# Performance work log

Hardware: AMD Instinct MI355X
Metric: run time of the kernel (lower is better)

The kernel has to match this reference:

```python
import jax, jax.numpy as jnp
import numpy as np
from jax import lax

D_MODEL = 256
N_LAYERS = 4
D_STATE = 64
EXPAND = 2
HEADDIM = 64
D_CONV = 4
D_INNER = EXPAND * D_MODEL                      # 512
NHEADS = D_INNER // HEADDIM                     # 8
CONV_DIM = D_INNER + 2 * D_STATE                # 640 (ngroups=1)
D_IN_PROJ = 2 * D_INNER + 2 * D_STATE + NHEADS  # 1160
B_SZ, SEQ = 8, 2048


def _silu(x):
    return x * jax.nn.sigmoid(x)


def _mamba2(u, W_in, W_conv, b_conv, dt_bias, A_log, Dp, norm_w, W_out):
    # Standard Mamba2 block (in_proj -> causal depthwise conv -> selective scan
    # with per-head scalar A -> gated RMSNorm -> out_proj).
    B, L, _ = u.shape
    zxbcdt = u @ W_in.T                                   # [B,L,1160]
    z = zxbcdt[..., :D_INNER]
    xBC = zxbcdt[..., D_INNER:D_INNER + CONV_DIM]
    dt = jax.nn.softplus(zxbcdt[..., D_INNER + CONV_DIM:] + dt_bias)  # [B,L,H]
    # causal depthwise conv1d + silu
    xc = lax.conv_general_dilated(xBC.transpose(0, 2, 1), W_conv[:, None, :],
                                  (1,), [(D_CONV - 1, 0)],
                                  dimension_numbers=('NCH', 'OIH', 'NCH'),
                                  feature_group_count=CONV_DIM)
    xBC = _silu(xc.transpose(0, 2, 1) + b_conv)
    x = xBC[..., :D_INNER].reshape(B, L, NHEADS, HEADDIM)
    Bm = xBC[..., D_INNER:D_INNER + D_STATE]              # [B,L,N]
    Cm = xBC[..., D_INNER + D_STATE:]                     # [B,L,N]
    dA = jnp.exp(dt * (-jnp.exp(A_log)))                  # [B,L,H]

    def step(h, inp):
        dA_t, dt_t, x_t, B_t, C_t = inp
        # h: [B,H,P,N]
        h = dA_t[:, :, None, None] * h + (dt_t[:, :, None] * x_t)[..., None] * B_t[:, None, None, :]
        y = jnp.einsum('bhpn,bn->bhp', h, C_t)
        return h, y

    h0 = jnp.zeros((B, NHEADS, HEADDIM, D_STATE), u.dtype)
    xs = (dA.transpose(1, 0, 2), dt.transpose(1, 0, 2), x.transpose(1, 0, 2, 3),
          Bm.transpose(1, 0, 2), Cm.transpose(1, 0, 2))
    _, ys = lax.scan(step, h0, xs)                        # [L,B,H,P]
    y = ys.transpose(1, 0, 2, 3) + Dp[None, None, :, None] * x
    y = y.reshape(B, L, D_INNER)
    y = y * _silu(z)                                      # gate before RMSNorm
    y = y * lax.rsqrt(jnp.mean(y * y, axis=-1, keepdims=True) + 1e-5) * norm_w
    return y @ W_out.T


def _encoder(x, pf, pb):
    for i in range(N_LAYERS - 1):
        y_fwd = _mamba2(x, *[p[i] for p in pf])
        y_bwd = _mamba2(x[:, ::-1], *[p[i] for p in pb])[:, ::-1]
        x = y_fwd + y_bwd
    h_fwd = _mamba2(x, *[p[-1] for p in pf])
    h_bwd = _mamba2(x[:, ::-1], *[p[-1] for p in pb])[:, ::-1]
    H = (h_fwd + h_bwd).mean(axis=1)
    return h_fwd, h_bwd, H


def _make_params(key):
    k = jax.random.split(key, 4)
    W_in = jax.random.normal(k[0], (N_LAYERS, D_IN_PROJ, D_MODEL), jnp.float32) * 0.02
    W_conv = jax.random.normal(k[1], (N_LAYERS, CONV_DIM, D_CONV), jnp.float32) * 0.2
    b_conv = jnp.zeros((N_LAYERS, CONV_DIM), jnp.float32)
    dt = jnp.exp(jax.random.uniform(k[2], (N_LAYERS, NHEADS)) * (np.log(0.1) - np.log(0.001)) + np.log(0.001))
    dt_bias = dt + jnp.log(-jnp.expm1(-dt))               # softplus^{-1}(dt)
    A_log = jnp.log(jax.random.uniform(k[3], (N_LAYERS, NHEADS), minval=1.0, maxval=16.0))
    Dp = jnp.ones((N_LAYERS, NHEADS), jnp.float32)
    norm_w = jnp.ones((N_LAYERS, D_INNER), jnp.float32)
    W_out = jax.random.normal(jax.random.fold_in(k[0], 7), (N_LAYERS, D_MODEL, D_INNER), jnp.float32) * 0.02
    return (W_in, W_conv, b_conv, dt_bias, A_log, Dp, norm_w, W_out)


def setup_inputs():
    key = jax.random.key(0)
    kx, kf, kb = jax.random.split(key, 3)
    x = jax.random.normal(kx, (B_SZ, SEQ, D_MODEL), jnp.float32)
    pf = _make_params(kf)
    pb = _make_params(kb)
    names = ['Win', 'Wconv', 'bconv', 'dt_bias', 'A_log', 'D', 'norm_w', 'Wout']
    inp = {'x_conditioned': x}
    for n, p in zip(names, pf):
        inp[n + '_f'] = p
    for n, p in zip(names, pb):
        inp[n + '_b'] = p
    return inp


def reference(x_conditioned, Win_f, Wconv_f, bconv_f, dt_bias_f, A_log_f, D_f, norm_w_f, Wout_f,
              Win_b, Wconv_b, bconv_b, dt_bias_b, A_log_b, D_b, norm_w_b, Wout_b):
    pf = (Win_f, Wconv_f, bconv_f, dt_bias_f, A_log_f, D_f, norm_w_f, Wout_f)
    pb = (Win_b, Wconv_b, bconv_b, dt_bias_b, A_log_b, D_b, norm_w_b, Wout_b)
    return _encoder(x_conditioned, pf, pb)
```

## Files before the change

### kernel.cpp

```cpp
#include <hip/hip_runtime.h>
#include <math.h>


#define TC 64
#define NC 32
#define SPITCH 72

#define ZB_STR   8388608u
#define XBCB_STR 10485760u
#define HINPU_STR 8388608u
#define XCP_STR  10485760u
#define DT_STR   131072u
#define SB_STR   131072u
#define PT_STR   2048u

typedef __attribute__((ext_vector_type(4))) float f32x4;
typedef __attribute__((ext_vector_type(8))) short s16x8;

#define MFMA __builtin_amdgcn_mfma_f32_16x16x32_bf16

__device__ __forceinline__ float siluf(float x) { return x / (1.f + expf(-x)); }

__device__ __forceinline__ ushort f2b(float f) {
  union { float f; uint u; } v; v.f = f;
  return (ushort)((v.u + 0x7FFFu + ((v.u >> 16) & 1u)) >> 16);
}
__device__ __forceinline__ float b2f(ushort u) {
  union { uint u; float f; } v; v.u = ((uint)u) << 16; return v.f;
}
__device__ __forceinline__ int swz(int r, int c) { return c ^ (r & 3) ^ ((r >> 2) & 3); }

__device__ __forceinline__ int soff(int base, int r, int cc) {
  return base + r * SPITCH + ((((cc >> 3) ^ (r & 7) ^ ((r >> 3) & 7)) << 3) | (cc & 7));
}
__device__ __forceinline__ int toff(int base, int r, int cc) {
  return base + r * 64 + ((((cc >> 3) ^ (r & 7)) << 3) | (cc & 7));
}

__device__ __forceinline__ uint packf(float y) {
  const ushort hb = f2b(y);
  const ushort lb = f2b(y - b2f(hb));
  return (uint)hb | ((uint)lb << 16);
}
__device__ __forceinline__ float unpackf(uint u) {
  return b2f((ushort)(u & 0xffffu)) + b2f((ushort)(u >> 16));
}

__device__ __forceinline__ void unzip8(const uint4 u0, const uint4 u1, s16x8& hh, s16x8& ll) {
  const uint a[8] = {u0.x, u0.y, u0.z, u0.w, u1.x, u1.y, u1.z, u1.w};
#pragma unroll
  for (int e = 0; e < 8; ++e) {
    hh[e] = (short)(a[e] & 0xffffu);
    ll[e] = (short)(a[e] >> 16);
  }
}

__device__ __forceinline__ void stage16p(ushort* tiles, const uint* src,
                                         int bh_, int bl_, int r, int c0) {
  const uint4 u0 = *(const uint4*)(src + c0);
  const uint4 u1 = *(const uint4*)(src + c0 + 4);
  const uint4 u2 = *(const uint4*)(src + c0 + 8);
  const uint4 u3 = *(const uint4*)(src + c0 + 12);
  s16x8 h0, l0, h1, l1;
  unzip8(u0, u1, h0, l0);
  unzip8(u2, u3, h1, l1);
  *(s16x8*)&tiles[toff(bh_, r, c0)]     = h0;
  *(s16x8*)&tiles[toff(bl_, r, c0)]     = l0;
  *(s16x8*)&tiles[toff(bh_, r, c0 + 8)] = h1;
  *(s16x8*)&tiles[toff(bl_, r, c0 + 8)] = l1;
}

__global__ __launch_bounds__(256) void k_cvt(
    const float* __restrict__ src, ushort* __restrict__ dst, int n8)
{
  const int i = blockIdx.x * 256 + threadIdx.x;
  if (i >= n8) return;
  const float4 v0 = *(const float4*)(src + (size_t)i * 8);
  const float4 v1 = *(const float4*)(src + (size_t)i * 8 + 4);
  s16x8 h;
#pragma unroll
  for (int e = 0; e < 4; ++e) h[e] = (short)f2b(((const float*)&v0)[e]);
#pragma unroll
  for (int e = 0; e < 4; ++e) h[e + 4] = (short)f2b(((const float*)&v1)[e]);
  *(s16x8*)(dst + (size_t)i * 8) = h;
}

__global__ __launch_bounds__(256) void k_gemmb(
    const ushort* __restrict__ A, const ushort* __restrict__ Winb, int layer,
    ushort* __restrict__ zb, ushort* __restrict__ xbc,
    const float* __restrict__ db0, const float* __restrict__ db1,
    const float* __restrict__ Al0, const float* __restrict__ Al1,
    float* __restrict__ dtb, float* __restrict__ dab)
{
  const int zd = blockIdx.z;
  const ushort* W = Winb + ((size_t)zd * 4 + layer) * 296960;
  zb  += (size_t)zd * ZB_STR;
  xbc += (size_t)zd * XBCB_STR;
  dtb += (size_t)zd * DT_STR;
  dab += (size_t)zd * DT_STR;
  const float* dt_bias = zd ? db1 : db0;
  const float* A_log   = zd ? Al1 : Al0;
  const int N = 1160, K = 256;

  __shared__ __align__(16) ushort lds[17408];
  const int tid = threadIdx.x;
  const int lane = tid & 63;
  const int wid = tid >> 6;
  const int wr = wid >> 1, wc = wid & 1;
  const int m0 = blockIdx.x * 128, n0 = blockIdx.y * 128;

  const int tr = tid >> 1;
  const int th = tid & 1;
  const int gm = m0 + tr;
  const int bb = gm >> 11, tt = gm & 2047;
  const int tphys = zd ? (2047 - tt) : tt;
  const ushort* Arow = A + (size_t)((bb << 11) + tphys) * 256 + th * 16;
  const int wn = n0 + tr;
  const ushort* Wrow = (wn < N) ? (W + (size_t)wn * K + th * 16) : nullptr;

  const int asw0 = tr * 32 + swz(tr, th * 2) * 8;
  const int asw1 = tr * 32 + swz(tr, th * 2 + 1) * 8;

  f32x4 acc[4][4];
#pragma unroll
  for (int i = 0; i < 4; ++i)
#pragma unroll
    for (int j = 0; j < 4; ++j) acc[i][j] = (f32x4){0.f, 0.f, 0.f, 0.f};

  int aoff[4], boff[4];
#pragma unroll
  for (int f = 0; f < 4; ++f) {
    const int ar = wr * 64 + f * 16 + (lane & 15);
    aoff[f] = ar * 32 + swz(ar, lane >> 4) * 8;
    const int br = wc * 64 + f * 16 + (lane & 15);
    boff[f] = 4096 + br * 32 + swz(br, lane >> 4) * 8;
  }

  const s16x8 zz = (s16x8){0, 0, 0, 0, 0, 0, 0, 0};
  s16x8 a0 = *(const s16x8*)(Arow);
  s16x8 a1 = *(const s16x8*)(Arow + 8);
  s16x8 b0 = zz, b1 = zz;
  if (Wrow) {
    b0 = *(const s16x8*)(Wrow);
    b1 = *(const s16x8*)(Wrow + 8);
  }

  for (int k0 = 0; k0 < K; k0 += 32) {
    __syncthreads();
    *(s16x8*)&lds[asw0] = a0;
    *(s16x8*)&lds[asw1] = a1;
    *(s16x8*)&lds[4096 + asw0] = b0;
    *(s16x8*)&lds[4096 + asw1] = b1;
    __syncthreads();
    if (k0 + 32 < K) {
      a0 = *(const s16x8*)(Arow + k0 + 32);
      a1 = *(const s16x8*)(Arow + k0 + 40);
      if (Wrow) {
        b0 = *(const s16x8*)(Wrow + k0 + 32);
        b1 = *(const s16x8*)(Wrow + k0 + 40);
      }
    }
    s16x8 af[4], bf[4];
#pragma unroll
    for (int f = 0; f < 4; ++f) {
      af[f] = *(const s16x8*)&lds[aoff[f]];
      bf[f] = *(const s16x8*)&lds[boff[f]];
    }
#pragma unroll
    for (int i = 0; i < 4; ++i)
#pragma unroll
      for (int j = 0; j < 4; ++j)
        acc[i][j] = MFMA(af[i], bf[j], acc[i][j], 0, 0, 0);
  }

  const int by = blockIdx.y;
  if (by == 9) {
    if (wc == 0 && (lane & 15) < 8) {
      const int cl = lane & 15;
      const float bias = dt_bias[cl];
      const float eAl = expf(A_log[cl]);
#pragma unroll
      for (int i = 0; i < 4; ++i) {
        const int r = m0 + wr * 64 + i * 16 + (lane >> 4) * 4;
#pragma unroll
        for (int g = 0; g < 4; ++g) {
          const float v = acc[i][0][g] + bias;
          const float sp = (v > 20.f) ? v : log1pf(expf(v));
          dtb[(size_t)(r + g) * 8 + cl] = sp;
          dab[(size_t)(r + g) * 8 + cl] = sp * eAl;
        }
      }
    }
    return;
  }
  __syncthreads();
#pragma unroll
  for (int i = 0; i < 4; ++i) {
    const int r = wr * 64 + i * 16 + (lane >> 4) * 4;
#pragma unroll
    for (int j = 0; j < 4; ++j) {
      const int ccol = wc * 64 + j * 16 + (lane & 15);
#pragma unroll
      for (int g = 0; g < 4; ++g)
        lds[(r + g) * 136 + ccol] = f2b(acc[i][j][g]);
    }
  }
  __syncthreads();
  const int rr = tid >> 1, hf = tid & 1;
  const int grow = m0 + rr;
  ushort* dst; int stride, colb;
  if (by < 4) { dst = zb;  stride = 512; colb = n0; }
  else        { dst = xbc; stride = 640; colb = n0 - 512; }
  ushort* dp = dst + (size_t)grow * stride + colb + hf * 64;
  const ushort* sp = &lds[rr * 136 + hf * 64];
#pragma unroll
  for (int q = 0; q < 8; ++q)
    *(s16x8*)(dp + q * 8) = *(const s16x8*)(sp + q * 8);
}

__global__ __launch_bounds__(256) void k_gemmo_mid(
    const ushort* __restrict__ ybf, const ushort* __restrict__ Woutb, int layer,
    ushort* __restrict__ xbf)
{
  __shared__ __align__(16) ushort lds[8192];
  const int tid = threadIdx.x;
  const int lane = tid & 63;
  const int wid = tid >> 6;
  const int wr = wid >> 1, wc = wid & 1;
  const int m0 = blockIdx.x * 128, n0 = blockIdx.y * 128;

  const int tr = tid >> 1;
  const int th = tid & 1;
  const int gm = m0 + tr;
  const int bb = gm >> 11, tt = gm & 2047;
  const int wn = n0 + tr;

  const int asw0 = tr * 32 + swz(tr, th * 2) * 8;
  const int asw1 = tr * 32 + swz(tr, th * 2 + 1) * 8;

  f32x4 acc[4][4];
#pragma unroll
  for (int i = 0; i < 4; ++i)
#pragma unroll
    for (int j = 0; j < 4; ++j) acc[i][j] = (f32x4){0.f, 0.f, 0.f, 0.f};

  int aoff[4], boff[4];
#pragma unroll
  for (int f = 0; f < 4; ++f) {
    const int ar = wr * 64 + f * 16 + (lane & 15);
    aoff[f] = ar * 32 + swz(ar, lane >> 4) * 8;
    const int br = wc * 64 + f * 16 + (lane & 15);
    boff[f] = 4096 + br * 32 + swz(br, lane >> 4) * 8;
  }

  for (int dir = 0; dir < 2; ++dir) {
    const int tphys = dir ? (2047 - tt) : tt;
    const ushort* Arow = ybf + (size_t)dir * ZB_STR
                       + (size_t)((bb << 11) + tphys) * 512 + th * 16;
    const ushort* Wrow = Woutb + ((size_t)dir * 4 + layer) * 131072
                       + (size_t)wn * 512 + th * 16;
    s16x8 a0 = *(const s16x8*)(Arow);
    s16x8 a1 = *(const s16x8*)(Arow + 8);
    s16x8 b0 = *(const s16x8*)(Wrow);
    s16x8 b1 = *(const s16x8*)(Wrow + 8);
    for (int k0 = 0; k0 < 512; k0 += 32) {
      __syncthreads();
      *(s16x8*)&lds[asw0] = a0;
      *(s16x8*)&lds[asw1] = a1;
      *(s16x8*)&lds[4096 + asw0] = b0;
      *(s16x8*)&lds[4096 + asw1] = b1;
      __syncthreads();
      if (k0 + 32 < 512) {
        a0 = *(const s16x8*)(Arow + k0 + 32);
        a1 = *(const s16x8*)(Arow + k0 + 40);
        b0 = *(const s16x8*)(Wrow + k0 + 32);
        b1 = *(const s16x8*)(Wrow + k0 + 40);
      }
      s16x8 af[4], bf[4];
#pragma unroll
      for (int f = 0; f < 4; ++f) {
        af[f] = *(const s16x8*)&lds[aoff[f]];
        bf[f] = *(const s16x8*)&lds[boff[f]];
      }
#pragma unroll
      for (int i = 0; i < 4; ++i)
#pragma unroll
        for (int j = 0; j < 4; ++j)
          acc[i][j] = MFMA(af[i], bf[j], acc[i][j], 0, 0, 0);
    }
  }

#pragma unroll
  for (int i = 0; i < 4; ++i) {
    const int rb = m0 + wr * 64 + i * 16 + (lane >> 4) * 4;
#pragma unroll
    for (int g = 0; g < 4; ++g) {
      const size_t rbase = (size_t)(rb + g) * 256 + n0 + wc * 64 + (lane & 15);
#pragma unroll
      for (int j = 0; j < 4; ++j)
        xbf[rbase + j * 16] = f2b(acc[i][j][g]);
    }
  }
}

__global__ __launch_bounds__(256) void k_gemmo_last(
    const ushort* __restrict__ ybf, const ushort* __restrict__ Woutb,
    float* __restrict__ hF, float* __restrict__ hB)
{
  const int zd = blockIdx.z;
  const ushort* A = ybf + (size_t)zd * ZB_STR;
  const ushort* W = Woutb + ((size_t)zd * 4 + 3) * 131072;
  float* Cout = zd ? hB : hF;

  __shared__ __align__(16) ushort lds[8192];
  const int tid = threadIdx.x;
  const int lane = tid & 63;
  const int wid = tid >> 6;
  const int wr = wid >> 1, wc = wid & 1;
  const int m0 = blockIdx.x * 128, n0 = blockIdx.y * 128;

  const int tr = tid >> 1;
  const int th = tid & 1;
  const int gm = m0 + tr;
  const ushort* Arow = A + (size_t)gm * 512 + th * 16;
  const int wn = n0 + tr;
  const ushort* Wrow = W + (size_t)wn * 512 + th * 16;

  const int asw0 = tr * 32 + swz(tr, th * 2) * 8;
  const int asw1 = tr * 32 + swz(tr, th * 2 + 1) * 8;

  f32x4 acc[4][4];
#pragma unroll
  for (int i = 0; i < 4; ++i)
#pragma unroll
    for (int j = 0; j < 4; ++j) acc[i][j] = (f32x4){0.f, 0.f, 0.f, 0.f};

  int aoff[4], boff[4];
#pragma unroll
  for (int f = 0; f < 4; ++f) {
    const int ar = wr * 64 + f * 16 + (lane & 15);
    aoff[f] = ar * 32 + swz(ar, lane >> 4) * 8;
    const int br = wc * 64 + f * 16 + (lane & 15);
    boff[f] = 4096 + br * 32 + swz(br, lane >> 4) * 8;
  }

  s16x8 a0 = *(const s16x8*)(Arow);
  s16x8 a1 = *(const s16x8*)(Arow + 8);
  s16x8 b0 = *(const s16x8*)(Wrow);
  s16x8 b1 = *(const s16x8*)(Wrow + 8);

  for (int k0 = 0; k0 < 512; k0 += 32) {
    __syncthreads();
    *(s16x8*)&lds[asw0] = a0;
    *(s16x8*)&lds[asw1] = a1;
    *(s16x8*)&lds[4096 + asw0] = b0;
    *(s16x8*)&lds[4096 + asw1] = b1;
    __syncthreads();
    if (k0 + 32 < 512) {
      a0 = *(const s16x8*)(Arow + k0 + 32);
      a1 = *(const s16x8*)(Arow + k0 + 40);
      b0 = *(const s16x8*)(Wrow + k0 + 32);
      b1 = *(const s16x8*)(Wrow + k0 + 40);
    }
    s16x8 af[4], bf[4];
#pragma unroll
    for (int f = 0; f < 4; ++f) {
      af[f] = *(const s16x8*)&lds[aoff[f]];
      bf[f] = *(const s16x8*)&lds[boff[f]];
    }
#pragma unroll
    for (int i = 0; i < 4; ++i)
#pragma unroll
      for (int j = 0; j < 4; ++j)
        acc[i][j] = MFMA(af[i], bf[j], acc[i][j], 0, 0, 0);
  }

#pragma unroll
  for (int i = 0; i < 4; ++i) {
    const int rb = m0 + wr * 64 + i * 16 + (lane >> 4) * 4;
#pragma unroll
    for (int g = 0; g < 4; ++g) {
      const int row = rb + g;
      const int b2_ = row >> 11, t2 = row & 2047;
      const int tw = zd ? (2047 - t2) : t2;
      float* crow = Cout + ((size_t)((b2_ << 11) + tw)) * 256 + n0 + wc * 64 + (lane & 15);
#pragma unroll
      for (int j = 0; j < 4; ++j)
        crow[j * 16] = acc[i][j][g];
    }
  }
}

__global__ __launch_bounds__(256) void k_conv(
    const ushort* __restrict__ xbc,
    const float* __restrict__ Wc0, const float* __restrict__ Wc1,
    const float* __restrict__ bc0, const float* __restrict__ bc1,
    uint* __restrict__ xcp)
{
  const int zd = blockIdx.z;
  xbc += (size_t)zd * XBCB_STR;
  xcp += (size_t)zd * XCP_STR;
  const float* Wc = zd ? Wc1 : Wc0;
  const float* bc = zd ? bc1 : bc0;

  const int t = threadIdx.x;
  const int cg = blockIdx.x * 8 + (t & 7);
  const int c0 = cg * 8;
  const int rt0 = (blockIdx.y * 32 + (t >> 3)) * 16;

  float4 wv[8];
  const float4* wp = (const float4*)(Wc + c0 * 4);
#pragma unroll
  for (int e = 0; e < 8; ++e) wv[e] = wp[e];
  float bias[8];
#pragma unroll
  for (int e = 0; e < 8; ++e) bias[e] = bc[c0 + e];

  const s16x8 zz = (s16x8){0, 0, 0, 0, 0, 0, 0, 0};
  s16x8 w0, w1, w2;
  {
    const int l0 = rt0 & 2047;
    w0 = (l0 >= 3) ? *(const s16x8*)(xbc + (size_t)(rt0 - 3) * 640 + c0) : zz;
    w1 = (l0 >= 2) ? *(const s16x8*)(xbc + (size_t)(rt0 - 2) * 640 + c0) : zz;
    w2 = (l0 >= 1) ? *(const s16x8*)(xbc + (size_t)(rt0 - 1) * 640 + c0) : zz;
  }

#pragma unroll 4
  for (int i = 0; i < 16; ++i) {
    const int row = rt0 + i;
    const s16x8 cur = *(const s16x8*)(xbc + (size_t)row * 640 + c0);
    uint o[8];
#pragma unroll
    for (int e = 0; e < 8; ++e) {
      const float* w = (const float*)&wv[e];
      float a = bias[e];
      a = fmaf(b2f((ushort)w0[e]), w[0], a);
      a = fmaf(b2f((ushort)w1[e]), w[1], a);
      a = fmaf(b2f((ushort)w2[e]), w[2], a);
      a = fmaf(b2f((ushort)cur[e]), w[3], a);
      o[e] = packf(siluf(a));
    }
    uint* op = xcp + (size_t)row * 640 + c0;
    *(uint4*)op = make_uint4(o[0], o[1], o[2], o[3]);
    *(uint4*)(op + 4) = make_uint4(o[4], o[5], o[6], o[7]);
    w0 = w1; w1 = w2; w2 = cur;
  }
}

__global__ __launch_bounds__(256) void k_scan1(
    uint* __restrict__ xcp, const float* __restrict__ dt,
    const float* __restrict__ dtA,
    const float* __restrict__ Dp0, const float* __restrict__ Dp1,
    uint* __restrict__ hin, float* __restrict__ Sbuf,
    float* __restrict__ PT)
{
  const int zd = blockIdx.z;
  xcp  += (size_t)zd * XCP_STR;
  dt   += (size_t)zd * DT_STR;
  dtA  += (size_t)zd * DT_STR;
  hin  += (size_t)zd * HINPU_STR;
  Sbuf += (size_t)zd * SB_STR;
  PT   += (size_t)zd * PT_STR;
  const float* Dp = zd ? Dp1 : Dp0;

  const int c = blockIdx.x & (NC - 1);
  const int bhi = blockIdx.x >> 5;
  const int b = bhi >> 3, h = bhi & 7;
  const int tid = threadIdx.x;
  const int lane = tid & 63;
  const int wid = tid >> 6;
  const int r0 = b * 2048 + c * TC;
  const int hbase = h * 64;
  __shared__ __align__(16) ushort tiles[24576];
  __shared__ float Ssh[64], dtsh[64], vsh[64];
  enum { PCH = 0, PCL = 4096, PBH = 8192, PBL = 12288, PXH = 16384, PXL = 20480 };

  if (tid < 64) {
    float a = dtA[(size_t)(r0 + tid) * 8 + h];
    const float d = dt[(size_t)(r0 + tid) * 8 + h];
#pragma unroll
    for (int off = 1; off < 64; off <<= 1) {
      const float t = __shfl_up(a, off);
      if (tid >= off) a += t;
    }
    const float slast = __shfl(a, 63);
    Ssh[tid] = a;
    dtsh[tid] = d;
    vsh[tid] = expf(a - slast) * d;
    Sbuf[(size_t)bhi * 2048 + c * TC + tid] = a;
    if (tid == 63) PT[bhi * NC + c] = expf(-slast);
  }
  {
    const int r = tid >> 2, c0 = (tid & 3) * 16;
    const uint* rowp = xcp + (size_t)(r0 + r) * 640;
    stage16p(tiles, rowp + 512, PBH, PBL, r, c0);
    stage16p(tiles, rowp + 576, PCH, PCL, r, c0);
    stage16p(tiles, rowp + hbase, PXH, PXL, r, c0);
  }
  __syncthreads();

  const int ib = wid * 16;
  const int frow = lane & 15;
  const int fkc = lane >> 4;

  const int tp = tid >> 2;
  const int tj0 = (tid & 3) * 16;
  s16x8 xtr[4], btr[4];
#pragma unroll
  for (int cc = 0; cc < 2; ++cc) {
    const int j0 = tj0 + cc * 8;
    s16x8 vh, vl, wh, wl;
#pragma unroll
    for (int e = 0; e < 8; ++e) {
      const int ax = toff(PXH, j0 + e, tp);
      vh[e] = (short)tiles[ax];
      vl[e] = (short)tiles[ax + 4096];
      const int ab = toff(PBH, j0 + e, tp);
      wh[e] = (short)tiles[ab];
      wl[e] = (short)tiles[ab + 4096];
    }
    xtr[cc] = vh; xtr[cc + 2] = vl;
    btr[cc] = wh; btr[cc + 2] = wl;
  }

  s16x8 pah[2], pal[2];
#pragma unroll
  for (int ks = 0; ks < 2; ++ks) {
    pah[ks] = *(const s16x8*)&tiles[toff(PCH, ib + frow, ks * 32 + fkc * 8)];
    pal[ks] = *(const s16x8*)&tiles[toff(PCL, ib + frow, ks * 32 + fkc * 8)];
  }
  f32x4 acc[4];
#pragma unroll
  for (int jt = 0; jt < 4; ++jt) acc[jt] = (f32x4){0.f, 0.f, 0.f, 0.f};
#pragma unroll
  for (int jt = 0; jt < 4; ++jt) {
#pragma unroll
    for (int ks = 0; ks < 2; ++ks) {
      const s16x8 tbh = *(const s16x8*)&tiles[toff(PBH, jt * 16 + frow, ks * 32 + fkc * 8)];
      const s16x8 tbl = *(const s16x8*)&tiles[toff(PBL, jt * 16 + frow, ks * 32 + fkc * 8)];
      acc[jt] = MFMA(pah[ks], tbh, acc[jt], 0, 0, 0);
      acc[jt] = MFMA(pah[ks], tbl, acc[jt], 0, 0, 0);
      acc[jt] = MFMA(pal[ks], tbh, acc[jt], 0, 0, 0);
    }
  }
  float Si[4];
#pragma unroll
  for (int g = 0; g < 4; ++g) Si[g] = Ssh[ib + fkc * 4 + g];
#pragma unroll
  for (int jt = 0; jt < 4; ++jt) {
    const int j = jt * 16 + frow;
    const float Sj = Ssh[j], dj = dtsh[j];
#pragma unroll
    for (int g = 0; g < 4; ++g) {
      const int i = ib + fkc * 4 + g;
      const float w = (j <= i) ? __expf(Sj - Si[g]) * dj : 0.f;
      const float gt = acc[jt][g] * w;
      const ushort gh = f2b(gt);
      tiles[toff(PCH, i, j)] = gh;
      tiles[toff(PCL, i, j)] = f2b(gt - b2f(gh));
    }
  }
  __syncthreads();

#pragma unroll
  for (int cc = 0; cc < 2; ++cc) {
    *(s16x8*)&tiles[toff(PXH, tp, tj0 + cc * 8)] = xtr[cc];
    *(s16x8*)&tiles[toff(PXL, tp, tj0 + cc * 8)] = xtr[cc + 2];
    *(s16x8*)&tiles[toff(PBH, tp, tj0 + cc * 8)] = btr[cc];
    *(s16x8*)&tiles[toff(PBL, tp, tj0 + cc * 8)] = btr[cc + 2];
  }
  __syncthreads();

  s16x8 gah[2], gal[2];
#pragma unroll
  for (int ks = 0; ks < 2; ++ks) {
    gah[ks] = *(const s16x8*)&tiles[toff(PCH, ib + frow, ks * 32 + fkc * 8)];
    gal[ks] = *(const s16x8*)&tiles[toff(PCL, ib + frow, ks * 32 + fkc * 8)];
  }
  const float dpv = Dp[h];
#pragma unroll
  for (int pt = 0; pt < 4; ++pt) {
    f32x4 accY = (f32x4){0.f, 0.f, 0.f, 0.f};
#pragma unroll
    for (int ks = 0; ks < 2; ++ks) {
      const s16x8 xh = *(const s16x8*)&tiles[toff(PXH, pt * 16 + frow, ks * 32 + fkc * 8)];
      const s16x8 xl = *(const s16x8*)&tiles[toff(PXL, pt * 16 + frow, ks * 32 + fkc * 8)];
      accY = MFMA(gah[ks], xh, accY, 0, 0, 0);
      accY = MFMA(gah[ks], xl, accY, 0, 0, 0);
      accY = MFMA(gal[ks], xh, accY, 0, 0, 0);
    }
    const int p = pt * 16 + frow;
#pragma unroll
    for (int g = 0; g < 4; ++g) {
      const int i = ib + fkc * 4 + g;
      const int ax = toff(PXH, p, i);
      const float xv = b2f(tiles[ax]) + b2f(tiles[ax + 4096]);
      xcp[(size_t)(r0 + i) * 640 + hbase + p] = packf(accY[g] + dpv * xv);
    }
  }

  s16x8 xvh[2], xvl[2];
#pragma unroll
  for (int ks = 0; ks < 2; ++ks) {
    const int J0 = ks * 32 + fkc * 8;
    const s16x8 xh = *(const s16x8*)&tiles[toff(PXH, ib + frow, J0)];
    const s16x8 xl = *(const s16x8*)&tiles[toff(PXL, ib + frow, J0)];
#pragma unroll
    for (int e = 0; e < 8; ++e) {
      const float xf = (b2f((ushort)xh[e]) + b2f((ushort)xl[e])) * vsh[J0 + e];
      const ushort nh = f2b(xf);
      xvh[ks][e] = (short)nh;
      xvl[ks][e] = (short)f2b(xf - b2f(nh));
    }
  }
  uint* hbp = hin + (((size_t)(bhi * NC + c)) << 12);
#pragma unroll
  for (int nt = 0; nt < 4; ++nt) {
    f32x4 accC = (f32x4){0.f, 0.f, 0.f, 0.f};
#pragma unroll
    for (int ks = 0; ks < 2; ++ks) {
      const s16x8 tbh = *(const s16x8*)&tiles[toff(PBH, nt * 16 + frow, ks * 32 + fkc * 8)];
      const s16x8 tbl = *(const s16x8*)&tiles[toff(PBL, nt * 16 + frow, ks * 32 + fkc * 8)];
      accC = MFMA(xvh[ks], tbh, accC, 0, 0, 0);
      accC = MFMA(xvh[ks], tbl, accC, 0, 0, 0);
      accC = MFMA(xvl[ks], tbh, accC, 0, 0, 0);
    }
    const int n = nt * 16 + frow;
    const int kss = nt >> 1;
    const int nlo3 = (n >> 3) & 3, ne = n & 7;
#pragma unroll
    for (int g = 0; g < 4; ++g) {
      const int plo = fkc * 4 + g;
      const int off = ((wid * 2 + kss) << 9) + (nlo3 * 16 + plo) * 8 + ne;
      hbp[off] = packf(accC[g]);
    }
  }
}

__global__ __launch_bounds__(256) void k_scan2(
    uint* __restrict__ hin, const float* __restrict__ PT)
{
  const int zd = blockIdx.z;
  hin += (size_t)zd * HINPU_STR;
  PT  += (size_t)zd * PT_STR;
  const int bh = blockIdx.x >> 2, jt = blockIdx.x & 3;
  const int t = threadIdx.x;
  float hv[4] = {0.f, 0.f, 0.f, 0.f};
  for (int c = 0; c < NC; ++c) {
    uint* base = hin + (((size_t)(bh * NC + c)) << 12) + (jt << 10) + t * 4;
    const float pt = PT[bh * NC + c];
    const uint4 u = *(const uint4*)base;
    const float vals[4] = {unpackf(u.x), unpackf(u.y), unpackf(u.z), unpackf(u.w)};
    uint4 nv;
    uint* nvp = (uint*)&nv;
#pragma unroll
    for (int k = 0; k < 4; ++k) {
      const float old = hv[k];
      hv[k] = fmaf(pt, hv[k], vals[k]);
      nvp[k] = packf(old);
    }
    *(uint4*)base = nv;
  }
}

__global__ __launch_bounds__(512) void k_scan3f(
    const uint* __restrict__ xcp, const ushort* __restrict__ z,
    const uint* __restrict__ hin, const float* __restrict__ Sbuf,
    const float* __restrict__ nw0, const float* __restrict__ nw1,
    ushort* __restrict__ ybf)
{
  const int zd = blockIdx.z;
  xcp  += (size_t)zd * XCP_STR;
  z    += (size_t)zd * ZB_STR;
  hin  += (size_t)zd * HINPU_STR;
  Sbuf += (size_t)zd * SB_STR;
  ybf  += (size_t)zd * ZB_STR;
  const float* normw = zd ? nw1 : nw0;

  const int c = blockIdx.x & (NC - 1);
  const int b = blockIdx.x >> 5;
  const int tid = threadIdx.x;
  const int lane = tid & 63;
  const int h = tid >> 6;
  const int r0 = b * 2048 + c * TC;
  const int frow = lane & 15;
  const int fk = (lane >> 4) * 8;
  __shared__ __align__(16) ushort ybuf[64 * 524];
  __shared__ float Esh[8][64];
  __shared__ float partial[64][9];
  __shared__ float scale[64];

  {
    const int r = tid >> 3, c0 = (tid & 7) * 8;
    const uint* rowp = xcp + (size_t)(r0 + r) * 640 + 576 + c0;
    const uint4 u0 = *(const uint4*)rowp;
    const uint4 u1 = *(const uint4*)(rowp + 4);
    s16x8 hh, ll;
    unzip8(u0, u1, hh, ll);
    *(s16x8*)&ybuf[soff(0, r, c0)]    = hh;
    *(s16x8*)&ybuf[soff(4608, r, c0)] = ll;
  }
  Esh[h][lane] = expf(-Sbuf[(size_t)((b * 8 + h) << 11) + c * TC + lane]);
  __syncthreads();

  const size_t cbase = ((size_t)((b * 8 + h) * NC + c)) << 12;
  s16x8 Bh[4][2], Bl[4][2];
  const uint* hb = hin + cbase + lane * 8;
#pragma unroll
  for (int jt = 0; jt < 4; ++jt)
#pragma unroll
    for (int ks = 0; ks < 2; ++ks) {
      const uint* p = hb + ((jt * 2 + ks) << 9);
      const uint4 u0 = *(const uint4*)p;
      const uint4 u1 = *(const uint4*)(p + 4);
      unzip8(u0, u1, Bh[jt][ks], Bl[jt][ks]);
    }
  s16x8 Ah[4][2], Al[4][2];
#pragma unroll
  for (int it = 0; it < 4; ++it)
#pragma unroll
    for (int ks = 0; ks < 2; ++ks) {
      Ah[it][ks] = *(const s16x8*)&ybuf[soff(0, it * 16 + frow, ks * 32 + fk)];
      Al[it][ks] = *(const s16x8*)&ybuf[soff(4608, it * 16 + frow, ks * 32 + fk)];
    }

  f32x4 acc[4][4];
#pragma unroll
  for (int it = 0; it < 4; ++it)
#pragma unroll
    for (int jt = 0; jt < 4; ++jt) acc[it][jt] = (f32x4){0.f, 0.f, 0.f, 0.f};
#pragma unroll
  for (int it = 0; it < 4; ++it)
#pragma unroll
    for (int jt = 0; jt < 4; ++jt)
#pragma unroll
      for (int ks = 0; ks < 2; ++ks) {
        acc[it][jt] = MFMA(Ah[it][ks], Bh[jt][ks], acc[it][jt], 0, 0, 0);
        acc[it][jt] = MFMA(Ah[it][ks], Bl[jt][ks], acc[it][jt], 0, 0, 0);
        acc[it][jt] = MFMA(Al[it][ks], Bh[jt][ks], acc[it][jt], 0, 0, 0);
      }

  float rowsq[4][4];
#pragma unroll
  for (int it = 0; it < 4; ++it)
#pragma unroll
    for (int g = 0; g < 4; ++g) rowsq[it][g] = 0.f;
#pragma unroll
  for (int it = 0; it < 4; ++it)
#pragma unroll
    for (int jt = 0; jt < 4; ++jt) {
      const int gcol = h * 64 + jt * 16 + frow;
#pragma unroll
      for (int g = 0; g < 4; ++g) {
        const int row = it * 16 + (lane >> 4) * 4 + g;
        const float yl = unpackf(xcp[(size_t)(r0 + row) * 640 + gcol]);
        const float zf = b2f(z[(size_t)(r0 + row) * 512 + gcol]);
        const float y = (yl + Esh[h][row] * acc[it][jt][g]) * siluf(zf);
        acc[it][jt][g] = y;
        rowsq[it][g] = fmaf(y, y, rowsq[it][g]);
      }
    }
#pragma unroll
  for (int it = 0; it < 4; ++it)
#pragma unroll
    for (int g = 0; g < 4; ++g) {
      float s = rowsq[it][g];
      s += __shfl_xor(s, 1);
      s += __shfl_xor(s, 2);
      s += __shfl_xor(s, 4);
      s += __shfl_xor(s, 8);
      if (frow == 0) partial[it * 16 + (lane >> 4) * 4 + g][h] = s;
    }
  __syncthreads();
  if (tid < 64) {
    float s = 0.f;
#pragma unroll
    for (int hh = 0; hh < 8; ++hh) s += partial[tid][hh];
    scale[tid] = rsqrtf(s * (1.f / 512.f) + 1e-5f);
  }
  __syncthreads();

  float wreg[4];
#pragma unroll
  for (int jt = 0; jt < 4; ++jt) wreg[jt] = normw[h * 64 + jt * 16 + frow];
#pragma unroll
  for (int it = 0; it < 4; ++it)
#pragma unroll
    for (int jt = 0; jt < 4; ++jt) {
      const int col = h * 64 + jt * 16 + frow;
#pragma unroll
      for (int g = 0; g < 4; ++g) {
        const int row = it * 16 + (lane >> 4) * 4 + g;
        ybuf[row * 524 + col] = f2b(acc[it][jt][g] * scale[row] * wreg[jt]);
      }
    }
  __syncthreads();
#pragma unroll
  for (int j = 0; j < 8; ++j) {
    const int flat = j * 4096 + tid * 8;
    const int row = flat >> 9, col = flat & 511;
    const ushort4 u0 = *(const ushort4*)&ybuf[row * 524 + col];
    const ushort4 u1 = *(const ushort4*)&ybuf[row * 524 + col + 4];
    s16x8 o;
    o[0] = (short)u0.x; o[1] = (short)u0.y; o[2] = (short)u0.z; o[3] = (short)u0.w;
    o[4] = (short)u1.x; o[5] = (short)u1.y; o[6] = (short)u1.z; o[7] = (short)u1.w;
    *(s16x8*)(ybf + (size_t)(r0 + row) * 512 + col) = o;
  }
}

__global__ __launch_bounds__(256) void k_hpart(
    const float* __restrict__ hf, const float* __restrict__ hb,
    float* __restrict__ part)
{
  const int g = blockIdx.x;
  const int b = g >> 5, seg = g & 31;
  const int m = threadIdx.x;
  float s = 0.f;
  for (int l = seg * 64; l < seg * 64 + 64; ++l) {
    const size_t idx = ((size_t)b * 2048 + l) * 256 + m;
    s += hf[idx] + hb[idx];
  }
  part[(size_t)g * 256 + m] = s;
}

__global__ __launch_bounds__(256) void k_hfinal(
    const float* __restrict__ part, float* __restrict__ H)
{
  const int b = blockIdx.x;
  const int m = threadIdx.x;
  float s = 0.f;
  for (int g = 0; g < 32; ++g) s += part[(size_t)(b * 32 + g) * 256 + m];
  H[b * 256 + m] = s * (1.f / 2048.f);
}

extern "C" void kernel_launch(void* const* d_in, const int* in_sizes, int n_in,
                              void* d_out, int out_size, void* d_ws, size_t ws_size,
                              hipStream_t stream) {
  const float* x_in = (const float*)d_in[0];
  const float* Win[2]    = {(const float*)d_in[1],  (const float*)d_in[9]};
  const float* Wconv[2]  = {(const float*)d_in[2],  (const float*)d_in[10]};
  const float* bconv[2]  = {(const float*)d_in[3],  (const float*)d_in[11]};
  const float* dtbias[2] = {(const float*)d_in[4],  (const float*)d_in[12]};
  const float* Alog[2]   = {(const float*)d_in[5],  (const float*)d_in[13]};
  const float* Dpar[2]   = {(const float*)d_in[6],  (const float*)d_in[14]};
  const float* normw[2]  = {(const float*)d_in[7],  (const float*)d_in[15]};
  const float* Wout[2]   = {(const float*)d_in[8],  (const float*)d_in[16]};

  float* ws = (float*)d_ws;
  ushort* zb    = (ushort*)ws;
  ushort* ybf   = zb;
  ushort* xbcb  = (ushort*)(ws + 8388608);
  uint* hinp    = (uint*)(ws + 18874368);
  uint* xcp     = (uint*)(ws + 35651584);
  float* dtb     = ws + 56623104;
  float* dab     = ws + 56885248;
  float* Sbuf    = ws + 57147392;
  float* PT      = ws + 57409536;
  float* part    = ws + 57413632;
  ushort* xbf    = (ushort*)(ws + 57479168);
  ushort* Winb   = (ushort*)(ws + 59576320);
  ushort* Woutb  = (ushort*)(ws + 60764160);

  float* hF = (float*)d_out;
  float* hB = hF + (size_t)8 * 2048 * 256;
  float* Hm = hB + (size_t)8 * 2048 * 256;

  k_cvt<<<580, 256, 0, stream>>>(Win[0], Winb, 148480);
  k_cvt<<<580, 256, 0, stream>>>(Win[1], Winb + 1187840, 148480);
  k_cvt<<<256, 256, 0, stream>>>(Wout[0], Woutb, 65536);
  k_cvt<<<256, 256, 0, stream>>>(Wout[1], Woutb + 524288, 65536);
  k_cvt<<<2048, 256, 0, stream>>>(x_in, xbf, 524288);

  for (int layer = 0; layer < 4; ++layer) {
    const float* Wc0 = Wconv[0] + (size_t)layer * 640 * 4;
    const float* Wc1 = Wconv[1] + (size_t)layer * 640 * 4;
    const float* bc0 = bconv[0] + (size_t)layer * 640;
    const float* bc1 = bconv[1] + (size_t)layer * 640;

    k_gemmb<<<dim3(128, 10, 2), 256, 0, stream>>>(
        xbf, Winb, layer, zb, xbcb,
        dtbias[0] + layer * 8, dtbias[1] + layer * 8,
        Alog[0] + layer * 8, Alog[1] + layer * 8, dtb, dab);
    k_conv<<<dim3(10, 32, 2), 256, 0, stream>>>(xbcb, Wc0, Wc1, bc0, bc1, xcp);
    k_scan1<<<dim3(2048, 1, 2), 256, 0, stream>>>(
        xcp, dtb, dab, Dpar[0] + layer * 8, Dpar[1] + layer * 8,
        hinp, Sbuf, PT);
    k_scan2<<<dim3(256, 1, 2), 256, 0, stream>>>(hinp, PT);
    k_scan3f<<<dim3(256, 1, 2), 512, 0, stream>>>(
        xcp, zb, hinp, Sbuf,
        normw[0] + layer * 512, normw[1] + layer * 512, ybf);
    if (layer < 3) {
      k_gemmo_mid<<<dim3(128, 2), 256, 0, stream>>>(ybf, Woutb, layer, xbf);
    } else {
      k_gemmo_last<<<dim3(128, 2, 2), 256, 0, stream>>>(ybf, Woutb, hF, hB);
    }
  }
  k_hpart<<<256, 256, 0, stream>>>(hF, hB, part);
  k_hfinal<<<8, 256, 0, stream>>>(part, Hm);
}
```

Measured before the change: 1.026 ms.

## Fuse x-channel causal conv and SiLU into scan1 tile staging

The depthwise conv now covers only the B/C channels (512..639), shrinking its grid. The scan1 kernel computes the conv plus SiLU for its head's 64 x channels directly from the bf16 in_proj output and splits the result into hi/lo bf16 parts straight into shared memory. This removes a write and re-read of the packed x activations through global memory. In exchange scan1 reads four input rows per output row and redoes conv arithmetic per block, and any later kernel that still reads x channels from xcp would see stale data.

```diff
diff --git a/kernel.cpp b/kernel.cpp
--- a/kernel.cpp
+++ b/kernel.cpp
@@ -405,7 +405,7 @@
 
   const int t = threadIdx.x;
   const int cg = blockIdx.x * 8 + (t & 7);
-  const int c0 = cg * 8;
+  const int c0 = 512 + cg * 8;
   const int rt0 = (blockIdx.y * 32 + (t >> 3)) * 16;
 
   float4 wv[8];
@@ -448,20 +448,25 @@
 }
 
 __global__ __launch_bounds__(256) void k_scan1(
-    uint* __restrict__ xcp, const float* __restrict__ dt,
-    const float* __restrict__ dtA,
+    uint* __restrict__ xcp, const ushort* __restrict__ xbcb,
+    const float* __restrict__ Wc0, const float* __restrict__ Wc1,
+    const float* __restrict__ bc0, const float* __restrict__ bc1,
+    const float* __restrict__ dt, const float* __restrict__ dtA,
     const float* __restrict__ Dp0, const float* __restrict__ Dp1,
     uint* __restrict__ hin, float* __restrict__ Sbuf,
     float* __restrict__ PT)
 {
   const int zd = blockIdx.z;
   xcp  += (size_t)zd * XCP_STR;
+  xbcb += (size_t)zd * XBCB_STR;
   dt   += (size_t)zd * DT_STR;
   dtA  += (size_t)zd * DT_STR;
   hin  += (size_t)zd * HINPU_STR;
   Sbuf += (size_t)zd * SB_STR;
   PT   += (size_t)zd * PT_STR;
   const float* Dp = zd ? Dp1 : Dp0;
+  const float* Wc = zd ? Wc1 : Wc0;
+  const float* bc = zd ? bc1 : bc0;
 
   const int c = blockIdx.x & (NC - 1);
   const int bhi = blockIdx.x >> 5;
@@ -491,11 +496,43 @@
     if (tid == 63) PT[bhi * NC + c] = expf(-slast);
   }
   {
-    const int r = tid >> 2, c0 = (tid & 3) * 16;
+    const int r = tid >> 2, c0q = (tid & 3) * 16;
     const uint* rowp = xcp + (size_t)(r0 + r) * 640;
-    stage16p(tiles, rowp + 512, PBH, PBL, r, c0);
-    stage16p(tiles, rowp + 576, PCH, PCL, r, c0);
-    stage16p(tiles, rowp + hbase, PXH, PXL, r, c0);
+    stage16p(tiles, rowp + 512, PBH, PBL, r, c0q);
+    stage16p(tiles, rowp + 576, PCH, PCL, r, c0q);
+
+    const int l = c * TC + r;
+    const ushort* xrow = xbcb + (size_t)(r0 + r) * 640 + hbase;
+#pragma unroll
+    for (int half = 0; half < 2; ++half) {
+      const int cc = c0q + half * 8;
+      float4 wv[8];
+      float accv[8];
+#pragma unroll
+      for (int e = 0; e < 8; ++e) {
+        wv[e] = *(const float4*)(Wc + (hbase + cc + e) * 4);
+        accv[e] = bc[hbase + cc + e];
+      }
+#pragma unroll
+      for (int k = 0; k < 4; ++k) {
+        if (l - 3 + k >= 0) {
+          const s16x8 v = *(const s16x8*)(xrow + (ptrdiff_t)(k - 3) * 640 + cc);
+#pragma unroll
+          for (int e = 0; e < 8; ++e)
+            accv[e] = fmaf(b2f((ushort)v[e]), ((const float*)&wv[e])[k], accv[e]);
+        }
+      }
+      s16x8 hh, ll;
+#pragma unroll
+      for (int e = 0; e < 8; ++e) {
+        const float sv = siluf(accv[e]);
+        const ushort hb2 = f2b(sv);
+        hh[e] = (short)hb2;
+        ll[e] = (short)f2b(sv - b2f(hb2));
+      }
+      *(s16x8*)&tiles[toff(PXH, r, cc)] = hh;
+      *(s16x8*)&tiles[toff(PXL, r, cc)] = ll;
+    }
   }
   __syncthreads();
 
@@ -881,9 +918,10 @@
         xbf, Winb, layer, zb, xbcb,
         dtbias[0] + layer * 8, dtbias[1] + layer * 8,
         Alog[0] + layer * 8, Alog[1] + layer * 8, dtb, dab);
-    k_conv<<<dim3(10, 32, 2), 256, 0, stream>>>(xbcb, Wc0, Wc1, bc0, bc1, xcp);
+    k_conv<<<dim3(2, 32, 2), 256, 0, stream>>>(xbcb, Wc0, Wc1, bc0, bc1, xcp);
     k_scan1<<<dim3(2048, 1, 2), 256, 0, stream>>>(
-        xcp, dtb, dab, Dpar[0] + layer * 8, Dpar[1] + layer * 8,
+        xcp, xbcb, Wc0, Wc1, bc0, bc1, dtb, dab,
+        Dpar[0] + layer * 8, Dpar[1] + layer * 8,
         hinp, Sbuf, PT);
     k_scan2<<<dim3(256, 1, 2), 256, 0, stream>>>(hinp, PT);
     k_scan3f<<<dim3(256, 1, 2), 512, 0, stream>>>(
```

Result: slower. 1.085 ms (+5.8%).
